# Kernel optimization log

Hardware: AMD Instinct MI355X
Metric: run time of the kernel (lower is better)

## Reference

```python
import jax, jax.numpy as jnp
import numpy as np

NUM_EXPERTS = 16
TOP_K = 4
N_GROUP = 4
TOPK_GROUP = 2
SCALING = 2.5


def setup_inputs() -> dict:
    key = jax.random.key(0)
    ks = jax.random.split(key, 9)
    B, S, H, I = 2, 1024, 2048, 1024
    w = lambda k, shape: jax.random.normal(k, shape, jnp.float32) * 0.02
    return {
        "hidden_states": jax.random.normal(ks[0], (B, S, H), jnp.float32),
        "gate_weight": w(ks[1], (NUM_EXPERTS, H)),
        "expert_bias": jnp.zeros((NUM_EXPERTS,), jnp.float32),
        "gate_proj": w(ks[2], (NUM_EXPERTS, I, H)),
        "up_proj": w(ks[3], (NUM_EXPERTS, I, H)),
        "down_proj": w(ks[4], (NUM_EXPERTS, H, I)),
        "shared_gate": w(ks[5], (I, H)),
        "shared_up": w(ks[6], (I, H)),
        "shared_down": w(ks[7], (H, I)),
    }


def _route(x, gate_weight, expert_bias):
    # x: [T, H] -> routing weights [T, K], selected experts [T, K]
    logits = x @ gate_weight.T                              # [T, E]
    scores = jax.nn.sigmoid(logits)
    biased = scores + expert_bias[None, :]                  # bias only for selection
    T = x.shape[0]
    gsz = NUM_EXPERTS // N_GROUP
    grp = biased.reshape(T, N_GROUP, gsz)
    top2, _ = jax.lax.top_k(grp, 2)
    group_scores = top2.sum(-1)                             # [T, G]
    _, gidx = jax.lax.top_k(group_scores, TOPK_GROUP)       # [T, topk_group]
    gmask = jax.nn.one_hot(gidx, N_GROUP, dtype=scores.dtype).sum(1)  # [T, G]
    emask = jnp.repeat(gmask, gsz, axis=1)                  # [T, E]
    masked = jnp.where(emask > 0, biased, -jnp.inf)
    _, sel = jax.lax.top_k(masked, TOP_K)                   # [T, K]
    w = jnp.take_along_axis(scores, sel, axis=1)            # weights from unbiased scores
    w = w / (w.sum(-1, keepdims=True) + 1e-20)              # norm_topk_prob
    return w * SCALING, sel


def _moe(x, w, sel, gate_proj, up_proj, down_proj):
    # combine weight per (token, expert): [T, E]; zero where expert not selected
    cw = (jax.nn.one_hot(sel, NUM_EXPERTS, dtype=x.dtype) * w[..., None]).sum(1)

    def body(acc, inp):
        g, u, d, we = inp                                   # g,u: [I,H]; d: [H,I]; we: [T]
        y = (jax.nn.silu(x @ g.T) * (x @ u.T)) @ d.T        # SwiGLU expert FFN
        return acc + we[:, None] * y, None

    out, _ = jax.lax.scan(body, jnp.zeros_like(x),
                          (gate_proj, up_proj, down_proj, cw.T))
    return out


def reference(hidden_states, gate_weight, expert_bias, gate_proj, up_proj,
              down_proj, shared_gate, shared_up, shared_down):
    B, S, H = hidden_states.shape
    x = hidden_states.reshape(-1, H)                        # [T, H]
    w, sel = _route(x, gate_weight, expert_bias)
    out = _moe(x, w, sel, gate_proj, up_proj, down_proj)
    shared = (jax.nn.silu(x @ shared_gate.T) * (x @ shared_up.T)) @ shared_down.T
    return (out + shared).reshape(B, S, H)
```

## Files before the change

kernel.cpp:

```cpp
#include <hip/hip_runtime.h>
#include <hip/hip_bf16.h>
#include <stdint.h>

#define T_TOK 2048
#define HDIM  2048
#define IDIM  1024
#define NEXP  16
#define SCALING 2.5f

typedef __attribute__((ext_vector_type(8))) short bf16x8;
typedef __attribute__((ext_vector_type(4))) float f32x4;

static __device__ __forceinline__ unsigned short f2bf(float f) {
    uint32_t u = __float_as_uint(f);
    u += 0x7FFF + ((u >> 16) & 1);
    return (unsigned short)(u >> 16);
}

#define GLD_LDS16(g, l) \
    __builtin_amdgcn_global_load_lds((const __attribute__((address_space(1))) uint32_t*)(g), \
                                     (__attribute__((address_space(3))) uint32_t*)(l), 16, 0, 0)

__global__ __launch_bounds__(256) void cvt_k(const float* __restrict__ x,
                                             unsigned short* __restrict__ o) {
    int i = (blockIdx.x * 256 + threadIdx.x) * 8;
    float4 f0 = *(const float4*)(x + i);
    float4 f1 = *(const float4*)(x + i + 4);
    union { unsigned short h[8]; uint4 v; } u;
    u.h[0] = f2bf(f0.x); u.h[1] = f2bf(f0.y); u.h[2] = f2bf(f0.z); u.h[3] = f2bf(f0.w);
    u.h[4] = f2bf(f1.x); u.h[5] = f2bf(f1.y); u.h[6] = f2bf(f1.z); u.h[7] = f2bf(f1.w);
    *(uint4*)(o + i) = u.v;
}

__global__ __launch_bounds__(256) void cvt_w1_k(const float* __restrict__ gate_w,
                                                const float* __restrict__ up_w,
                                                const float* __restrict__ shg,
                                                const float* __restrict__ shu,
                                                unsigned short* __restrict__ wbf1) {
    size_t flat = ((size_t)blockIdx.x * 256 + threadIdx.x) * 8;
    int e   = (int)(flat >> 22);
    int rem = (int)(flat & ((1u << 22) - 1));
    int row = rem >> 11;
    int h   = rem & 2047;
    int f   = row >> 1;
    const float* src;
    if (e == NEXP) src = (row & 1) ? shu : shg;
    else           src = ((row & 1) ? up_w : gate_w) + (size_t)e * (IDIM * HDIM);
    src += (size_t)f * HDIM + h;
    float4 f0 = *(const float4*)src;
    float4 f1 = *(const float4*)(src + 4);
    union { unsigned short s[8]; uint4 v; } u;
    u.s[0] = f2bf(f0.x); u.s[1] = f2bf(f0.y); u.s[2] = f2bf(f0.z); u.s[3] = f2bf(f0.w);
    u.s[4] = f2bf(f1.x); u.s[5] = f2bf(f1.y); u.s[6] = f2bf(f1.z); u.s[7] = f2bf(f1.w);
    *(uint4*)(wbf1 + flat) = u.v;
}

__global__ __launch_bounds__(256) void cvt_w2_k(const float* __restrict__ down_w,
                                                const float* __restrict__ shd,
                                                unsigned short* __restrict__ wbf2) {
    size_t flat = ((size_t)blockIdx.x * 256 + threadIdx.x) * 8;
    int e   = (int)(flat >> 21);
    int rem = (int)(flat & ((1u << 21) - 1));
    const float* src = (e == NEXP) ? shd : (down_w + (size_t)e * (HDIM * IDIM));
    src += rem;
    float4 f0 = *(const float4*)src;
    float4 f1 = *(const float4*)(src + 4);
    union { unsigned short s[8]; uint4 v; } u;
    u.s[0] = f2bf(f0.x); u.s[1] = f2bf(f0.y); u.s[2] = f2bf(f0.z); u.s[3] = f2bf(f0.w);
    u.s[4] = f2bf(f1.x); u.s[5] = f2bf(f1.y); u.s[6] = f2bf(f1.z); u.s[7] = f2bf(f1.w);
    *(uint4*)(wbf2 + flat) = u.v;
}

__global__ __launch_bounds__(256) void route_k(const float* __restrict__ x,
                                               const float* __restrict__ gw,
                                               const float* __restrict__ bias,
                                               int* __restrict__ tokl,
                                               float* __restrict__ twl,
                                               int* __restrict__ cnt) {
    __shared__ float slog[NEXP];
    int t = blockIdx.x;
    int tid = threadIdx.x;
    int e = tid >> 4, r = tid & 15;
    const float* xp = x + (size_t)t * HDIM;
    const float* wp = gw + (size_t)e * HDIM;
    float p = 0.f;
    for (int j = r; j < HDIM; j += 16) p += xp[j] * wp[j];
    for (int off = 8; off; off >>= 1) p += __shfl_down(p, off, 16);
    if (r == 0) slog[e] = p;
    __syncthreads();
    if (tid == 0) {
        float sc[NEXP], bi[NEXP];
        for (int i = 0; i < NEXP; i++) {
            sc[i] = 1.f / (1.f + expf(-slog[i]));
            bi[i] = sc[i] + bias[i];
        }
        float gsc[4];
        for (int g = 0; g < 4; g++) {
            float v0 = bi[g*4+0], v1 = bi[g*4+1], v2 = bi[g*4+2], v3 = bi[g*4+3];
            float hi01 = fmaxf(v0, v1), lo01 = fminf(v0, v1);
            float hi23 = fmaxf(v2, v3), lo23 = fminf(v2, v3);
            float top1 = fmaxf(hi01, hi23);
            float sec  = fmaxf(fminf(hi01, hi23), (hi01 >= hi23) ? lo01 : lo23);
            gsc[g] = top1 + sec;
        }
        int g0 = 0; for (int g = 1; g < 4; g++) if (gsc[g] > gsc[g0]) g0 = g;
        int g1 = (g0 == 0) ? 1 : 0;
        for (int g = 0; g < 4; g++) if (g != g0 && gsc[g] > gsc[g1]) g1 = g;
        float mk[NEXP];
        for (int i = 0; i < NEXP; i++) {
            int gg = i >> 2;
            mk[i] = (gg == g0 || gg == g1) ? bi[i] : -INFINITY;
        }
        int sel[4]; float wv[4]; float wsum = 0.f;
        for (int k = 0; k < 4; k++) {
            int bmax = 0; float bv = -INFINITY;
            for (int i = 0; i < NEXP; i++) if (mk[i] > bv) { bv = mk[i]; bmax = i; }
            sel[k] = bmax; mk[bmax] = -INFINITY;
            wv[k] = sc[bmax]; wsum += sc[bmax];
        }
        float scale = SCALING / (wsum + 1e-20f);
        for (int k = 0; k < 4; k++) {
            int ee = sel[k];
            int slot = atomicAdd(&cnt[ee], 1);
            tokl[ee * T_TOK + slot] = t;
            twl[ee * T_TOK + slot] = wv[k] * scale;
        }
    }
}

__global__ __launch_bounds__(512, 2) void gemm1_k(const unsigned short* __restrict__ Xbf,
                                                  const unsigned short* __restrict__ wbf1,
                                                  const int* __restrict__ tokl,
                                                  const int* __restrict__ cnt,
                                                  unsigned short* __restrict__ act) {
    extern __shared__ unsigned short sm[];
    int b = blockIdx.x;
    int swz = (b & 7) * 136 + (b >> 3);
    int e = swz >> 6, mt = (swz >> 3) & 7, nt = swz & 7;
    int C = (e == NEXP) ? T_TOK : cnt[e];
    int m0 = mt * 256;
    if (m0 >= C) return;
    int tid = threadIdx.x;

    int c8 = tid & 7, rr = tid >> 3;
    int swzc = c8 ^ (rr & 7);
    const char* aA[4];
    const char* aB[4];
#pragma unroll
    for (int i = 0; i < 4; i++) {
        int slot = m0 + i * 64 + rr;
        int sl = (slot < C) ? slot : (C - 1);
        int tk = (e == NEXP) ? sl : tokl[e * T_TOK + sl];
        aA[i] = (const char*)Xbf + ((size_t)tk * HDIM + (size_t)swzc * 8) * 2;
        int brow = nt * 256 + i * 64 + rr;
        aB[i] = (const char*)wbf1 + (((size_t)e << 22) + (size_t)brow * HDIM + (size_t)swzc * 8) * 2;
    }

    int lane = tid & 63, wid = tid >> 6;
    int wm = wid >> 2, wn = wid & 3;
    int fr = lane & 15, kg = lane >> 4;
    int xo = fr & 7;

    f32x4 acc[8][4];
#pragma unroll
    for (int m = 0; m < 8; m++)
#pragma unroll
        for (int n = 0; n < 4; n++) acc[m][n] = (f32x4){0.f, 0.f, 0.f, 0.f};

    auto stage = [&](int kt, int bf) {
        size_t kb = (size_t)kt * 128;
        char* dA = (char*)(sm + bf * 16384);
        char* dB = (char*)(sm + 32768 + bf * 16384);
#pragma unroll
        for (int i = 0; i < 4; i++) GLD_LDS16(aA[i] + kb, dA + i * 8192 + tid * 16);
#pragma unroll
        for (int i = 0; i < 4; i++) GLD_LDS16(aB[i] + kb, dB + i * 8192 + tid * 16);
    };

    stage(0, 0);
    asm volatile("s_waitcnt vmcnt(0)" ::: "memory");
    __builtin_amdgcn_s_barrier();

    const int NT = 32;
    for (int kt = 0; kt < NT; ++kt) {
        int bf = kt & 1;
        __builtin_amdgcn_s_barrier();
        __builtin_amdgcn_sched_barrier(0);
        if (kt + 1 < NT) {
            stage(kt + 1, bf ^ 1);
            asm volatile("s_waitcnt vmcnt(8)" ::: "memory");
        } else {
            asm volatile("s_waitcnt vmcnt(0)" ::: "memory");
        }
        __builtin_amdgcn_s_barrier();
        __builtin_amdgcn_sched_barrier(0);

        const char* lA = (const char*)(sm + bf * 16384);
        const char* lB = (const char*)(sm + 32768 + bf * 16384);
        bf16x8 bv[4][2];
#pragma unroll
        for (int n = 0; n < 4; n++)
#pragma unroll
            for (int h = 0; h < 2; h++)
                bv[n][h] = *(const bf16x8*)(lB + (wn * 64 + n * 16 + fr) * 128 + ((((h << 2) | kg) ^ xo) << 4));
#pragma unroll
        for (int p = 0; p < 4; p++) {
            bf16x8 av[2][2];
#pragma unroll
            for (int mm = 0; mm < 2; mm++)
#pragma unroll
                for (int h = 0; h < 2; h++)
                    av[mm][h] = *(const bf16x8*)(lA + (wm * 128 + (p * 2 + mm) * 16 + fr) * 128 + ((((h << 2) | kg) ^ xo) << 4));
            asm volatile("s_waitcnt lgkmcnt(0)" ::: "memory");
            __builtin_amdgcn_sched_barrier(0);
            __builtin_amdgcn_s_setprio(1);
#pragma unroll
            for (int h = 0; h < 2; h++)
#pragma unroll
                for (int n = 0; n < 4; n++) {
                    acc[p * 2 + 0][n] = __builtin_amdgcn_mfma_f32_16x16x32_bf16(av[0][h], bv[n][h], acc[p * 2 + 0][n], 0, 0, 0);
                    acc[p * 2 + 1][n] = __builtin_amdgcn_mfma_f32_16x16x32_bf16(av[1][h], bv[n][h], acc[p * 2 + 1][n], 0, 0, 0);
                }
            __builtin_amdgcn_s_setprio(0);
        }
    }

    unsigned short* actE = act + (size_t)e * T_TOK * IDIM;
#pragma unroll
    for (int m = 0; m < 8; m++)
#pragma unroll
        for (int n = 0; n < 4; n++)
#pragma unroll
            for (int q = 0; q < 4; q++) {
                float v = acc[m][n][q];
                float pu = __shfl_xor(v, 1, 64);
                int slot = m0 + wm * 128 + m * 16 + kg * 4 + q;
                if (!(lane & 1) && slot < C) {
                    float g = v, u = pu;
                    float a = g / (1.f + __expf(-g)) * u;
                    int j = nt * 128 + wn * 32 + n * 8 + (fr >> 1);
                    actE[(size_t)slot * IDIM + j] = f2bf(a);
                }
            }
}

__global__ __launch_bounds__(512, 2) void gemm2_k(const unsigned short* __restrict__ act,
                                                  const unsigned short* __restrict__ wbf2,
                                                  const int* __restrict__ tokl,
                                                  const float* __restrict__ twl,
                                                  const int* __restrict__ cnt,
                                                  float* __restrict__ out) {
    extern __shared__ unsigned short sm[];
    int b = blockIdx.x;
    int swz = (b & 7) * 136 + (b >> 3);
    int e = swz >> 6, mt = (swz >> 3) & 7, nt = swz & 7;
    int C = (e == NEXP) ? T_TOK : cnt[e];
    int m0 = mt * 256;
    if (m0 >= C) return;
    int nb = nt * 256;
    int tid = threadIdx.x;

    const unsigned short* actE = act + (size_t)e * T_TOK * IDIM;
    int c8 = tid & 7, rr = tid >> 3;
    int swzc = c8 ^ (rr & 7);
    const char* aA[4];
    const char* aB[4];
#pragma unroll
    for (int i = 0; i < 4; i++) {
        int slot = m0 + i * 64 + rr;
        aA[i] = (const char*)actE + ((size_t)slot * IDIM + (size_t)swzc * 8) * 2;
        aB[i] = (const char*)wbf2 + (((size_t)e << 21) + (size_t)(nb + i * 64 + rr) * IDIM + (size_t)swzc * 8) * 2;
    }

    int lane = tid & 63, wid = tid >> 6;
    int wm = wid >> 2, wn = wid & 3;
    int fr = lane & 15, kg = lane >> 4;
    int xo = fr & 7;

    f32x4 acc[8][4];
#pragma unroll
    for (int m = 0; m < 8; m++)
#pragma unroll
        for (int n = 0; n < 4; n++) acc[m][n] = (f32x4){0.f, 0.f, 0.f, 0.f};

    auto stage = [&](int kt, int bf) {
        size_t kb = (size_t)kt * 128;
        char* dA = (char*)(sm + bf * 16384);
        char* dB = (char*)(sm + 32768 + bf * 16384);
#pragma unroll
        for (int i = 0; i < 4; i++) GLD_LDS16(aA[i] + kb, dA + i * 8192 + tid * 16);
#pragma unroll
        for (int i = 0; i < 4; i++) GLD_LDS16(aB[i] + kb, dB + i * 8192 + tid * 16);
    };

    stage(0, 0);
    asm volatile("s_waitcnt vmcnt(0)" ::: "memory");
    __builtin_amdgcn_s_barrier();

    const int NT = 16;
    for (int kt = 0; kt < NT; ++kt) {
        int bf = kt & 1;
        __builtin_amdgcn_s_barrier();
        __builtin_amdgcn_sched_barrier(0);
        if (kt + 1 < NT) {
            stage(kt + 1, bf ^ 1);
            asm volatile("s_waitcnt vmcnt(8)" ::: "memory");
        } else {
            asm volatile("s_waitcnt vmcnt(0)" ::: "memory");
        }
        __builtin_amdgcn_s_barrier();
        __builtin_amdgcn_sched_barrier(0);

        const char* lA = (const char*)(sm + bf * 16384);
        const char* lB = (const char*)(sm + 32768 + bf * 16384);
        bf16x8 bv[4][2];
#pragma unroll
        for (int n = 0; n < 4; n++)
#pragma unroll
            for (int h = 0; h < 2; h++)
                bv[n][h] = *(const bf16x8*)(lB + (wn * 64 + n * 16 + fr) * 128 + ((((h << 2) | kg) ^ xo) << 4));
#pragma unroll
        for (int p = 0; p < 4; p++) {
            bf16x8 av[2][2];
#pragma unroll
            for (int mm = 0; mm < 2; mm++)
#pragma unroll
                for (int h = 0; h < 2; h++)
                    av[mm][h] = *(const bf16x8*)(lA + (wm * 128 + (p * 2 + mm) * 16 + fr) * 128 + ((((h << 2) | kg) ^ xo) << 4));
            asm volatile("s_waitcnt lgkmcnt(0)" ::: "memory");
            __builtin_amdgcn_sched_barrier(0);
            __builtin_amdgcn_s_setprio(1);
#pragma unroll
            for (int h = 0; h < 2; h++)
#pragma unroll
                for (int n = 0; n < 4; n++) {
                    acc[p * 2 + 0][n] = __builtin_amdgcn_mfma_f32_16x16x32_bf16(av[0][h], bv[n][h], acc[p * 2 + 0][n], 0, 0, 0);
                    acc[p * 2 + 1][n] = __builtin_amdgcn_mfma_f32_16x16x32_bf16(av[1][h], bv[n][h], acc[p * 2 + 1][n], 0, 0, 0);
                }
            __builtin_amdgcn_s_setprio(0);
        }
    }

#pragma unroll
    for (int m = 0; m < 8; m++)
#pragma unroll
        for (int q = 0; q < 4; q++) {
            int slot = m0 + wm * 128 + m * 16 + kg * 4 + q;
            if (slot >= C) continue;
            int tk; float wg;
            if (e == NEXP) { tk = slot; wg = 1.f; }
            else { tk = tokl[e * T_TOK + slot]; wg = twl[e * T_TOK + slot]; }
            float* o = out + (size_t)tk * HDIM + nb + wn * 64 + fr;
#pragma unroll
            for (int n = 0; n < 4; n++)
                atomicAdd(o + n * 16, wg * acc[m][n][q]);
        }
}

extern "C" void kernel_launch(void* const* d_in, const int* in_sizes, int n_in,
                              void* d_out, int out_size, void* d_ws, size_t ws_size,
                              hipStream_t stream) {
    const float* x      = (const float*)d_in[0];
    const float* gw     = (const float*)d_in[1];
    const float* bias   = (const float*)d_in[2];
    const float* gate_w = (const float*)d_in[3];
    const float* up_w   = (const float*)d_in[4];
    const float* down_w = (const float*)d_in[5];
    const float* shg    = (const float*)d_in[6];
    const float* shu    = (const float*)d_in[7];
    const float* shd    = (const float*)d_in[8];
    float* out = (float*)d_out;
    char* ws = (char*)d_ws;

    unsigned short* Xbf  = (unsigned short*)ws;
    unsigned short* act  = (unsigned short*)(ws + 8388608ULL);
    unsigned short* wbf1 = (unsigned short*)(ws + 79691776ULL);
    unsigned short* wbf2 = (unsigned short*)(ws + 222298112ULL);
    int*            tokl = (int*)(ws + 293601280ULL);
    float*          twl  = (float*)(ws + 293732352ULL);
    int*            cnt  = (int*)(ws + 293863424ULL);

    static bool attr_set = false;
    if (!attr_set) {
        hipFuncSetAttribute((const void*)gemm1_k, hipFuncAttributeMaxDynamicSharedMemorySize, 131072);
        hipFuncSetAttribute((const void*)gemm2_k, hipFuncAttributeMaxDynamicSharedMemorySize, 131072);
        attr_set = true;
    }

    hipMemsetAsync(out, 0, (size_t)out_size * 4, stream);
    hipMemsetAsync(cnt, 0, 64, stream);
    cvt_k<<<2048, 256, 0, stream>>>(x, Xbf);
    cvt_w1_k<<<34816, 256, 0, stream>>>(gate_w, up_w, shg, shu, wbf1);
    cvt_w2_k<<<17408, 256, 0, stream>>>(down_w, shd, wbf2);
    route_k<<<2048, 256, 0, stream>>>(x, gw, bias, tokl, twl, cnt);
    gemm1_k<<<1088, 512, 131072, stream>>>(Xbf, wbf1, tokl, cnt, act);
    gemm2_k<<<1088, 512, 131072, stream>>>(act, wbf2, tokl, twl, cnt, out);
}
```

Before: 901.3 us.

## Replace atomic scatter with bf16 partials and gather-reduce; fuse convert kernels

```diff
diff --git a/kernel.cpp b/kernel.cpp
--- a/kernel.cpp
+++ b/kernel.cpp
@@ -21,70 +21,70 @@
     __builtin_amdgcn_global_load_lds((const __attribute__((address_space(1))) uint32_t*)(g), \
                                      (__attribute__((address_space(3))) uint32_t*)(l), 16, 0, 0)
 
-__global__ __launch_bounds__(256) void cvt_k(const float* __restrict__ x,
-                                             unsigned short* __restrict__ o) {
-    int i = (blockIdx.x * 256 + threadIdx.x) * 8;
-    float4 f0 = *(const float4*)(x + i);
-    float4 f1 = *(const float4*)(x + i + 4);
-    union { unsigned short h[8]; uint4 v; } u;
-    u.h[0] = f2bf(f0.x); u.h[1] = f2bf(f0.y); u.h[2] = f2bf(f0.z); u.h[3] = f2bf(f0.w);
-    u.h[4] = f2bf(f1.x); u.h[5] = f2bf(f1.y); u.h[6] = f2bf(f1.z); u.h[7] = f2bf(f1.w);
-    *(uint4*)(o + i) = u.v;
-}
-
-__global__ __launch_bounds__(256) void cvt_w1_k(const float* __restrict__ gate_w,
-                                                const float* __restrict__ up_w,
-                                                const float* __restrict__ shg,
-                                                const float* __restrict__ shu,
-                                                unsigned short* __restrict__ wbf1) {
-    size_t flat = ((size_t)blockIdx.x * 256 + threadIdx.x) * 8;
-    int e   = (int)(flat >> 22);
-    int rem = (int)(flat & ((1u << 22) - 1));
-    int row = rem >> 11;
-    int h   = rem & 2047;
-    int f   = row >> 1;
+__global__ __launch_bounds__(256) void cvtw_k(const float* __restrict__ gate_w,
+                                              const float* __restrict__ up_w,
+                                              const float* __restrict__ shg,
+                                              const float* __restrict__ shu,
+                                              const float* __restrict__ down_w,
+                                              const float* __restrict__ shd,
+                                              unsigned short* __restrict__ wbf1,
+                                              unsigned short* __restrict__ wbf2) {
+    int b = blockIdx.x;
     const float* src;
-    if (e == NEXP) src = (row & 1) ? shu : shg;
-    else           src = ((row & 1) ? up_w : gate_w) + (size_t)e * (IDIM * HDIM);
-    src += (size_t)f * HDIM + h;
+    unsigned short* dst;
+    size_t flat;
+    if (b < 34816) {
+        flat = ((size_t)b * 256 + threadIdx.x) * 8;
+        int e   = (int)(flat >> 22);
+        int rem = (int)(flat & ((1u << 22) - 1));
+        int row = rem >> 11;
+        int h   = rem & 2047;
+        int f   = row >> 1;
+        if (e == NEXP) src = (row & 1) ? shu : shg;
+        else           src = ((row & 1) ? up_w : gate_w) + (size_t)e * (IDIM * HDIM);
+        src += (size_t)f * HDIM + h;
+        dst = wbf1 + flat;
+    } else {
+        flat = ((size_t)(b - 34816) * 256 + threadIdx.x) * 8;
+        int e   = (int)(flat >> 21);
+        int rem = (int)(flat & ((1u << 21) - 1));
+        src = ((e == NEXP) ? shd : (down_w + (size_t)e * (HDIM * IDIM))) + rem;
+        dst = wbf2 + flat;
+    }
     float4 f0 = *(const float4*)src;
     float4 f1 = *(const float4*)(src + 4);
     union { unsigned short s[8]; uint4 v; } u;
     u.s[0] = f2bf(f0.x); u.s[1] = f2bf(f0.y); u.s[2] = f2bf(f0.z); u.s[3] = f2bf(f0.w);
     u.s[4] = f2bf(f1.x); u.s[5] = f2bf(f1.y); u.s[6] = f2bf(f1.z); u.s[7] = f2bf(f1.w);
-    *(uint4*)(wbf1 + flat) = u.v;
-}
-
-__global__ __launch_bounds__(256) void cvt_w2_k(const float* __restrict__ down_w,
-                                                const float* __restrict__ shd,
-                                                unsigned short* __restrict__ wbf2) {
-    size_t flat = ((size_t)blockIdx.x * 256 + threadIdx.x) * 8;
-    int e   = (int)(flat >> 21);
-    int rem = (int)(flat & ((1u << 21) - 1));
-    const float* src = (e == NEXP) ? shd : (down_w + (size_t)e * (HDIM * IDIM));
-    src += rem;
-    float4 f0 = *(const float4*)src;
-    float4 f1 = *(const float4*)(src + 4);
-    union { unsigned short s[8]; uint4 v; } u;
-    u.s[0] = f2bf(f0.x); u.s[1] = f2bf(f0.y); u.s[2] = f2bf(f0.z); u.s[3] = f2bf(f0.w);
-    u.s[4] = f2bf(f1.x); u.s[5] = f2bf(f1.y); u.s[6] = f2bf(f1.z); u.s[7] = f2bf(f1.w);
-    *(uint4*)(wbf2 + flat) = u.v;
-}
-
-__global__ __launch_bounds__(256) void route_k(const float* __restrict__ x,
-                                               const float* __restrict__ gw,
-                                               const float* __restrict__ bias,
-                                               int* __restrict__ tokl,
-                                               float* __restrict__ twl,
-                                               int* __restrict__ cnt) {
+    *(uint4*)dst = u.v;
+}
+
+__global__ __launch_bounds__(256) void route2_k(const float* __restrict__ x,
+                                                const float* __restrict__ gw,
+                                                const float* __restrict__ bias,
+                                                unsigned short* __restrict__ Xbf,
+                                                int* __restrict__ tokl,
+                                                float* __restrict__ twl,
+                                                int* __restrict__ cnt,
+                                                int* __restrict__ sl4) {
+    __shared__ float sx[HDIM];
     __shared__ float slog[NEXP];
     int t = blockIdx.x;
     int tid = threadIdx.x;
+    const float* xp = x + (size_t)t * HDIM;
+    float4 f0 = *(const float4*)(xp + tid * 8);
+    float4 f1 = *(const float4*)(xp + tid * 8 + 4);
+    union { unsigned short h[8]; uint4 v; } u;
+    u.h[0] = f2bf(f0.x); u.h[1] = f2bf(f0.y); u.h[2] = f2bf(f0.z); u.h[3] = f2bf(f0.w);
+    u.h[4] = f2bf(f1.x); u.h[5] = f2bf(f1.y); u.h[6] = f2bf(f1.z); u.h[7] = f2bf(f1.w);
+    *(uint4*)(Xbf + (size_t)t * HDIM + tid * 8) = u.v;
+    *(float4*)(sx + tid * 8) = f0;
+    *(float4*)(sx + tid * 8 + 4) = f1;
+    __syncthreads();
     int e = tid >> 4, r = tid & 15;
-    const float* xp = x + (size_t)t * HDIM;
     const float* wp = gw + (size_t)e * HDIM;
     float p = 0.f;
-    for (int j = r; j < HDIM; j += 16) p += xp[j] * wp[j];
+    for (int j = r; j < HDIM; j += 16) p += sx[j] * wp[j];
     for (int off = 8; off; off >>= 1) p += __shfl_down(p, off, 16);
     if (r == 0) slog[e] = p;
     __syncthreads();
@@ -124,6 +124,7 @@
             int slot = atomicAdd(&cnt[ee], 1);
             tokl[ee * T_TOK + slot] = t;
             twl[ee * T_TOK + slot] = wv[k] * scale;
+            sl4[t * 4 + k] = ee * T_TOK + slot;
         }
     }
 }
@@ -236,8 +237,8 @@
                 float pu = __shfl_xor(v, 1, 64);
                 int slot = m0 + wm * 128 + m * 16 + kg * 4 + q;
                 if (!(lane & 1) && slot < C) {
-                    float g = v, u = pu;
-                    float a = g / (1.f + __expf(-g)) * u;
+                    float g = v, u2 = pu;
+                    float a = g / (1.f + __expf(-g)) * u2;
                     int j = nt * 128 + wn * 32 + n * 8 + (fr >> 1);
                     actE[(size_t)slot * IDIM + j] = f2bf(a);
                 }
@@ -246,10 +247,9 @@
 
 __global__ __launch_bounds__(512, 2) void gemm2_k(const unsigned short* __restrict__ act,
                                                   const unsigned short* __restrict__ wbf2,
-                                                  const int* __restrict__ tokl,
                                                   const float* __restrict__ twl,
                                                   const int* __restrict__ cnt,
-                                                  float* __restrict__ out) {
+                                                  unsigned short* __restrict__ part) {
     extern __shared__ unsigned short sm[];
     int b = blockIdx.x;
     int swz = (b & 7) * 136 + (b >> 3);
@@ -347,14 +347,39 @@
         for (int q = 0; q < 4; q++) {
             int slot = m0 + wm * 128 + m * 16 + kg * 4 + q;
             if (slot >= C) continue;
-            int tk; float wg;
-            if (e == NEXP) { tk = slot; wg = 1.f; }
-            else { tk = tokl[e * T_TOK + slot]; wg = twl[e * T_TOK + slot]; }
-            float* o = out + (size_t)tk * HDIM + nb + wn * 64 + fr;
+            float wg = (e == NEXP) ? 1.f : twl[e * T_TOK + slot];
+            unsigned short* pr = part + (size_t)(e * T_TOK + slot) * HDIM + nb + wn * 64 + fr;
 #pragma unroll
             for (int n = 0; n < 4; n++)
-                atomicAdd(o + n * 16, wg * acc[m][n][q]);
-        }
+                pr[n * 16] = f2bf(wg * acc[m][n][q]);
+        }
+}
+
+__global__ __launch_bounds__(256) void reduce_k(const unsigned short* __restrict__ part,
+                                                const int* __restrict__ sl4,
+                                                float* __restrict__ out) {
+    int t = blockIdx.x;
+    int h = threadIdx.x * 8;
+    int4 s = *(const int4*)(sl4 + t * 4);
+    const unsigned short* p0 = part + (size_t)s.x * HDIM + h;
+    const unsigned short* p1 = part + (size_t)s.y * HDIM + h;
+    const unsigned short* p2 = part + (size_t)s.z * HDIM + h;
+    const unsigned short* p3 = part + (size_t)s.w * HDIM + h;
+    const unsigned short* p4 = part + (size_t)(NEXP * T_TOK + t) * HDIM + h;
+    float o[8];
+#pragma unroll
+    for (int i = 0; i < 8; i++) o[i] = 0.f;
+    auto addv = [&](const unsigned short* p) {
+        uint4 a = *(const uint4*)p;
+        const unsigned short* q = (const unsigned short*)&a;
+#pragma unroll
+        for (int i = 0; i < 8; i++) o[i] += __uint_as_float((uint32_t)q[i] << 16);
+    };
+    addv(p0); addv(p1); addv(p2); addv(p3); addv(p4);
+    float4 r0 = {o[0], o[1], o[2], o[3]};
+    float4 r1 = {o[4], o[5], o[6], o[7]};
+    *(float4*)(out + (size_t)t * HDIM + h) = r0;
+    *(float4*)(out + (size_t)t * HDIM + h + 4) = r1;
 }
 
 extern "C" void kernel_launch(void* const* d_in, const int* in_sizes, int n_in,
@@ -379,6 +404,8 @@
     int*            tokl = (int*)(ws + 293601280ULL);
     float*          twl  = (float*)(ws + 293732352ULL);
     int*            cnt  = (int*)(ws + 293863424ULL);
+    int*            sl4  = (int*)(ws + 293863488ULL);
+    unsigned short* part = wbf1;
 
     static bool attr_set = false;
     if (!attr_set) {
@@ -387,12 +414,10 @@
         attr_set = true;
     }
 
-    hipMemsetAsync(out, 0, (size_t)out_size * 4, stream);
     hipMemsetAsync(cnt, 0, 64, stream);
-    cvt_k<<<2048, 256, 0, stream>>>(x, Xbf);
-    cvt_w1_k<<<34816, 256, 0, stream>>>(gate_w, up_w, shg, shu, wbf1);
-    cvt_w2_k<<<17408, 256, 0, stream>>>(down_w, shd, wbf2);
-    route_k<<<2048, 256, 0, stream>>>(x, gw, bias, tokl, twl, cnt);
+    cvtw_k<<<52224, 256, 0, stream>>>(gate_w, up_w, shg, shu, down_w, shd, wbf1, wbf2);
+    route2_k<<<2048, 256, 0, stream>>>(x, gw, bias, Xbf, tokl, twl, cnt, sl4);
     gemm1_k<<<1088, 512, 131072, stream>>>(Xbf, wbf1, tokl, cnt, act);
-    gemm2_k<<<1088, 512, 131072, stream>>>(act, wbf2, tokl, twl, cnt, out);
-}
+    gemm2_k<<<1088, 512, 131072, stream>>>(act, wbf2, twl, cnt, part);
+    reduce_k<<<2048, 256, 0, stream>>>(part, sl4, out);
+}
```

Measured after the change: 843.9 us. 1.07x faster.
